# Optimization experiments

Measured on AMD Instinct MI355X. Metric: run time of the kernel, lower is better.

## Reference

```python
import jax, jax.numpy as jnp
import numpy as np

E4M3_MAX = 448.0  # fp8_max_fwd for Format.HYBRID fprop tensors
MARGIN = 0        # DelayedScaling default


def _quantize_e4m3(t, s):
    # cast_to_fp8: scale, saturate-cast to E4M3; amax of the unscaled tensor
    q = (t * s).astype(jnp.float8_e4m3fn)
    amax = jnp.max(jnp.abs(t))
    return q, amax


def _sf_compute(amax, scale, fp8_max, margin):
    # faithful port of _default_sf_compute (including its tf.where ordering)
    exp = jnp.floor(jnp.log2(fp8_max / amax)) - margin
    sf = jnp.round(jnp.exp2(jnp.abs(exp)))
    sf = jnp.where(amax > 0.0, sf, scale)
    sf = jnp.where(jnp.isinf(amax), sf, scale)
    sf = jnp.where(exp < 0, 1.0 / sf, sf)
    return sf


def setup_inputs() -> dict:
    key = jax.random.key(0)
    k1, k2 = jax.random.split(key)
    M, K, N = 16384, 2048, 2048
    x = jax.random.normal(k1, (M, K), dtype=jnp.float32)
    kernel = jax.random.normal(k2, (K, N), dtype=jnp.float32) * 0.02
    scale = jnp.ones((2,), dtype=jnp.float32)
    scale_inv = jnp.ones((2,), dtype=jnp.float32)
    amax_history = jnp.zeros((1, 2), dtype=jnp.float32)
    return {"x": x, "kernel": kernel, "scale": scale,
            "scale_inv": scale_inv, "amax_history": amax_history}


def reference(x, kernel, scale, scale_inv, amax_history):
    # --- cast_to_fp8 for activation (index 0) and weight (index 1) ---
    x_q, amax_x = _quantize_e4m3(x, scale[0])          # [M, K] fp8
    w_q, amax_w = _quantize_e4m3(kernel.T, scale[1])   # [N, K] fp8 (B in row-major, gemm does B^T)
    new_scale_inv = jnp.stack([1.0 / scale[0], 1.0 / scale[1]])
    # record amaxes into most-recent slot of the history
    amax_history = amax_history.at[0, 0].set(amax_x).at[0, 1].set(amax_w)

    # --- fp8_matmul: D = (A * A_scale_inv) @ (B * B_scale_inv)^T ---
    out = jnp.matmul(x_q.astype(jnp.float32), w_q.astype(jnp.float32).T)
    out = out * (new_scale_inv[0] * new_scale_inv[1])  # [M, N]

    # --- fused_amax_and_scale_update (amax_compute_algo='most_recent') ---
    amax = amax_history[0]
    rolled = jnp.roll(amax_history, -1, axis=0).at[0].set(0.0)
    new_scale = _sf_compute(amax, scale, E4M3_MAX, MARGIN)
    return out, new_scale, rolled
```

## Files before the change

### kernel.cpp

```cpp
#include <hip/hip_runtime.h>
#include <cstdint>

#define M_DIM 16384
#define K_DIM 2048
#define N_DIM 2048

typedef float f32x4 __attribute__((ext_vector_type(4)));
typedef int   i32x8 __attribute__((ext_vector_type(8)));

__global__ __launch_bounds__(256) void quant_x_kernel(
    const float4* __restrict__ x, uint4* __restrict__ xq,
    const float* __restrict__ scale, unsigned int* __restrict__ amax)
{
    const int gid = blockIdx.x * 256 + threadIdx.x;
    const float s = scale[0];
    float m = 0.0f;
#pragma unroll
    for (int j = 0; j < 8; ++j) {
        float4 v = x[gid + j * 1048576];
        m = fmaxf(m, fmaxf(fmaxf(fabsf(v.x), fabsf(v.y)),
                           fmaxf(fabsf(v.z), fabsf(v.w))));
        unsigned int p0 = __builtin_amdgcn_cvt_pk_fp8_f32(v.x * s, v.y * s, 0, false);
        unsigned int p  = __builtin_amdgcn_cvt_pk_fp8_f32(v.z * s, v.w * s, p0, true);
        ((unsigned int*)xq)[gid + j * 1048576] = p;
    }

#pragma unroll
    for (int off = 32; off > 0; off >>= 1)
        m = fmaxf(m, __shfl_down(m, off, 64));
    __shared__ float red[4];
    if ((threadIdx.x & 63) == 0) red[threadIdx.x >> 6] = m;
    __syncthreads();
    if (threadIdx.x == 0) {
        m = fmaxf(fmaxf(red[0], red[1]), fmaxf(red[2], red[3]));
        atomicMax(amax, __float_as_uint(m));
    }
}

__global__ __launch_bounds__(256) void quant_w_kernel(
    const float* __restrict__ w, uint8_t* __restrict__ wq,
    const float* __restrict__ scale, unsigned int* __restrict__ amax)
{
    __shared__ float tile[64][68];
    const int t = threadIdx.x;
    const int nb = blockIdx.x * 64;
    const int kb = blockIdx.y * 64;
    const float s = scale[1];
    float m = 0.0f;
#pragma unroll
    for (int j = 0; j < 4; ++j) {
        int f = j * 256 + t;
        int row = f >> 4;
        int c4 = f & 15;
        float4 v = *(const float4*)(w + (size_t)(kb + row) * N_DIM + nb + c4 * 4);
        m = fmaxf(m, fmaxf(fmaxf(fabsf(v.x), fabsf(v.y)),
                           fmaxf(fabsf(v.z), fabsf(v.w))));
        *(float4*)(&tile[row][c4 * 4]) = v;
    }
    __syncthreads();
    const int n = t >> 2, c = t & 3;
    unsigned int pk[4];
#pragma unroll
    for (int jj = 0; jj < 4; ++jj) {
        float f0 = tile[c * 16 + jj * 4 + 0][n] * s;
        float f1 = tile[c * 16 + jj * 4 + 1][n] * s;
        float f2 = tile[c * 16 + jj * 4 + 2][n] * s;
        float f3 = tile[c * 16 + jj * 4 + 3][n] * s;
        unsigned int p = __builtin_amdgcn_cvt_pk_fp8_f32(f0, f1, 0, false);
        pk[jj] = __builtin_amdgcn_cvt_pk_fp8_f32(f2, f3, p, true);
    }
    *(uint4*)(wq + (size_t)(nb + n) * K_DIM + kb + c * 16) = make_uint4(pk[0], pk[1], pk[2], pk[3]);

#pragma unroll
    for (int off = 32; off > 0; off >>= 1)
        m = fmaxf(m, __shfl_down(m, off, 64));
    __shared__ float red[4];
    if ((t & 63) == 0) red[t >> 6] = m;
    __syncthreads();
    if (t == 0) {
        m = fmaxf(fmaxf(red[0], red[1]), fmaxf(red[2], red[3]));
        atomicMax(amax, __float_as_uint(m));
    }
}

#define LDSBUF 32768

__global__ __launch_bounds__(512, 2) void gemm_fp8_kernel(
    const uint8_t* __restrict__ Aq, const uint8_t* __restrict__ Bq,
    const float* __restrict__ scale, float* __restrict__ C)
{
    extern __shared__ uint8_t lds[];
    uint8_t* const lA = lds;
    uint8_t* const lB = lds + 2 * LDSBUF;

    const int tid  = threadIdx.x;
    const int wave = tid >> 6;
    const int lane = tid & 63;
    const int wm = wave >> 2, wn = wave & 3;
    const int q = lane >> 4, r = lane & 15;

    const int bn = blockIdx.x;
    const int bm = blockIdx.y;

    const float s0 = scale[0];
    const float s1 = scale[1];
    asm volatile("s_waitcnt vmcnt(0) lgkmcnt(0)" ::: "memory");

    const int seg = wave & 1;
    const int wp  = wave >> 1;
    const int gbB = wp + ((wp >> 1) << 1);
    const int npr = seg * 64 + lane;
    const int nin = npr ^ ((npr >> 3) & 1);
    const int srow = (nin >> 1) & 15;
    const int skb  = (((nin >> 1) >> 4) << 5) + ((nin & 1) << 4);
    const int sdst = seg * 1024 + lane * 16;

    const uint8_t* aS = Aq + (size_t)(bm * 256 + srow) * K_DIM + skb;
    const uint8_t* bS = Bq + (size_t)(bn * 256 + srow) * K_DIM + skb;

#define STAGE_A(buf, kb, g)                                                          \
    __builtin_amdgcn_global_load_lds(                                                \
        (const __attribute__((address_space(1))) uint32_t*)(aS + (size_t)(g) * (16 * K_DIM) + (kb)), \
        (__attribute__((address_space(3))) uint32_t*)(lA + (buf) * LDSBUF + (g) * 2048 + sdst), 16, 0, 0)
#define STAGE_B(buf, kb, g)                                                          \
    __builtin_amdgcn_global_load_lds(                                                \
        (const __attribute__((address_space(1))) uint32_t*)(bS + (size_t)(g) * (16 * K_DIM) + (kb)), \
        (__attribute__((address_space(3))) uint32_t*)(lB + (buf) * LDSBUF + (g) * 2048 + sdst), 16, 0, 0)

    const int sb   = (lane >> 2) & 1;
    const int offL = (((lane << 1) ^ sb) << 4);
    const int offH = ((((lane << 1) + 1) ^ sb) << 4);

    f32x4 acc[8][4];
#pragma unroll
    for (int i = 0; i < 8; ++i)
#pragma unroll
        for (int j = 0; j < 4; ++j) acc[i][j] = (f32x4){0.f, 0.f, 0.f, 0.f};

    STAGE_A(0, 0, wp);       STAGE_A(0, 0, 8 + wp);
    STAGE_B(0, 0, gbB);      STAGE_B(0, 0, 8 + gbB);
    STAGE_B(0, 0, 2 + gbB);  STAGE_B(0, 0, 10 + gbB);
    STAGE_A(0, 0, 4 + wp);   STAGE_A(0, 0, 12 + wp);
    asm volatile("s_waitcnt vmcnt(4)" ::: "memory");
    __builtin_amdgcn_s_barrier();

    const int SONE = 0x7F7F7F7F;

#pragma unroll 2
    for (int t = 0; t < 16; ++t) {
        const int cur = t & 1, nxt = cur ^ 1;
        const int kbn = ((t + 1) & 15) * 128;
        uint8_t* const curA = lA + cur * LDSBUF;
        uint8_t* const curB = lB + cur * LDSBUF;
        i32x8 a_frag[4];
#pragma unroll
        for (int p = 0; p < 4; ++p) {
            const int mh = p >> 1, nh = p & 1;
            if (nh == 0) {
#pragma unroll
                for (int mi = 0; mi < 4; ++mi) {
                    const uint8_t* pa = curA + (wm * 8 + mh * 4 + mi) * 2048;
                    int4 lo = *(const int4*)(pa + offL);
                    int4 hi = *(const int4*)(pa + offH);
                    a_frag[mi] = (i32x8){lo.x, lo.y, lo.z, lo.w,
                                         hi.x, hi.y, hi.z, hi.w};
                }
            }
            i32x8 b_frag[2];
#pragma unroll
            for (int j = 0; j < 2; ++j) {
                const uint8_t* pb = curB + (wn * 4 + nh * 2 + j) * 2048;
                int4 lo = *(const int4*)(pb + offL);
                int4 hi = *(const int4*)(pb + offH);
                b_frag[j] = (i32x8){lo.x, lo.y, lo.z, lo.w,
                                    hi.x, hi.y, hi.z, hi.w};
            }
            if (p == 0)      { STAGE_A(nxt, kbn, wp);       STAGE_A(nxt, kbn, 8 + wp); }
            else if (p == 1) { STAGE_B(nxt, kbn, gbB);      STAGE_B(nxt, kbn, 8 + gbB); }
            else if (p == 2) { STAGE_B(nxt, kbn, 2 + gbB);  STAGE_B(nxt, kbn, 10 + gbB); }
            else             { STAGE_A(nxt, kbn, 4 + wp);   STAGE_A(nxt, kbn, 12 + wp); }

            if (p != 2) asm volatile("s_waitcnt vmcnt(4)" ::: "memory");
            __builtin_amdgcn_s_barrier();
            asm volatile("s_waitcnt lgkmcnt(0)" ::: "memory");
            __builtin_amdgcn_sched_barrier(0);
            __builtin_amdgcn_s_setprio(1);
#pragma unroll
            for (int mi = 0; mi < 4; ++mi)
#pragma unroll
                for (int j = 0; j < 2; ++j)
                    acc[mh * 4 + mi][nh * 2 + j] =
                        __builtin_amdgcn_mfma_scale_f32_16x16x128_f8f6f4(
                            a_frag[mi], b_frag[j], acc[mh * 4 + mi][nh * 2 + j],
                            0 , 0 ,
                            0, SONE, 0, SONE);
            __builtin_amdgcn_s_setprio(0);
            __builtin_amdgcn_s_barrier();
        }
    }
#undef STAGE_A
#undef STAGE_B

    const float sinv = (1.0f / s0) * (1.0f / s1);
#pragma unroll
    for (int mi = 0; mi < 8; ++mi) {
#pragma unroll
        for (int ni = 0; ni < 4; ++ni) {
            const int col  = bn * 256 + wn * 64 + ni * 16 + r;
            const int row0 = bm * 256 + wm * 128 + mi * 16 + q * 4;
#pragma unroll
            for (int rr = 0; rr < 4; ++rr)
                C[(size_t)(row0 + rr) * N_DIM + col] = acc[mi][ni][rr] * sinv;
        }
    }
}

__global__ void finalize_kernel(const float* __restrict__ scale,
                                const unsigned int* __restrict__ amax_bits,
                                float* __restrict__ out_tail)
{
    const int i = threadIdx.x;
    if (i < 2) {
        const float amax = __uint_as_float(amax_bits[i]);
        const float sc = scale[i];
        const float e = floorf(log2f(448.0f / amax));
        float sf = roundf(exp2f(fabsf(e)));
        sf = (amax > 0.0f) ? sf : sc;
        sf = isinf(amax) ? sf : sc;
        if (e < 0.0f) sf = 1.0f / sf;
        out_tail[i] = sf;
        out_tail[2 + i] = 0.0f;
    }
}

extern "C" void kernel_launch(void* const* d_in, const int* in_sizes, int n_in,
                              void* d_out, int out_size, void* d_ws, size_t ws_size,
                              hipStream_t stream)
{
    const float* x     = (const float*)d_in[0];
    const float* w     = (const float*)d_in[1];
    const float* scale = (const float*)d_in[2];

    uint8_t* ws = (uint8_t*)d_ws;
    uint8_t* xq = ws;
    uint8_t* wq = ws + (size_t)M_DIM * K_DIM;
    unsigned int* amax = (unsigned int*)(ws + (size_t)M_DIM * K_DIM + (size_t)N_DIM * K_DIM);

    static int lds_opt_in = 0;
    if (!lds_opt_in) {
        hipFuncSetAttribute((const void*)gemm_fp8_kernel,
                            hipFuncAttributeMaxDynamicSharedMemorySize, 131072);
        lds_opt_in = 1;
    }

    hipMemsetAsync(amax, 0, 2 * sizeof(unsigned int), stream);

    quant_x_kernel<<<4096, 256, 0, stream>>>(
        (const float4*)x, (uint4*)xq, scale, amax);

    dim3 gw(N_DIM / 64, K_DIM / 64);
    quant_w_kernel<<<gw, 256, 0, stream>>>(w, wq, scale, amax + 1);

    dim3 gg(N_DIM / 256, M_DIM / 256);
    gemm_fp8_kernel<<<gg, 512, 131072, stream>>>(xq, wq, scale, (float*)d_out);

    finalize_kernel<<<1, 64, 0, stream>>>(scale, amax,
                                          (float*)d_out + (size_t)M_DIM * N_DIM);
}
```

Baseline: 376.6 us.

## Restructure fp8 GEMM pipeline, add XCD-aware tile mapping, widen quant stores

Reorganizes the GEMM main loop: all next-tile loads are issued up front, and the four compute phases are split with finer vmcnt waits and fewer barriers. This reduces synchronization stalls. Blocks use a 1D grid remapped so each XCD gets contiguous M-tiles, to improve L2 reuse of B. The activation quantization now packs 16 values per thread into one 128-bit store, doubling the grid. The hand-tuned vmcnt counts risk subtle races if they are miscounted.

New measurement: 848.4 us. 125% more time.

```diff
diff --git a/kernel.cpp b/kernel.cpp
--- a/kernel.cpp
+++ b/kernel.cpp
@@ -14,16 +14,21 @@
 {
     const int gid = blockIdx.x * 256 + threadIdx.x;
     const float s = scale[0];
+    float4 vv[4];
+#pragma unroll
+    for (int j = 0; j < 4; ++j) vv[j] = x[gid * 4 + j];
+
     float m = 0.0f;
-#pragma unroll
-    for (int j = 0; j < 8; ++j) {
-        float4 v = x[gid + j * 1048576];
+    unsigned int pks[4];
+#pragma unroll
+    for (int j = 0; j < 4; ++j) {
+        float4 v = vv[j];
         m = fmaxf(m, fmaxf(fmaxf(fabsf(v.x), fabsf(v.y)),
                            fmaxf(fabsf(v.z), fabsf(v.w))));
         unsigned int p0 = __builtin_amdgcn_cvt_pk_fp8_f32(v.x * s, v.y * s, 0, false);
-        unsigned int p  = __builtin_amdgcn_cvt_pk_fp8_f32(v.z * s, v.w * s, p0, true);
-        ((unsigned int*)xq)[gid + j * 1048576] = p;
-    }
+        pks[j] = __builtin_amdgcn_cvt_pk_fp8_f32(v.z * s, v.w * s, p0, true);
+    }
+    xq[gid] = make_uint4(pks[0], pks[1], pks[2], pks[3]);
 
 #pragma unroll
     for (int off = 32; off > 0; off >>= 1)
@@ -99,8 +104,10 @@
     const int wm = wave >> 2, wn = wave & 3;
     const int q = lane >> 4, r = lane & 15;
 
-    const int bn = blockIdx.x;
-    const int bm = blockIdx.y;
+    const int id  = blockIdx.x;
+    const int xcd = id & 7, idx = id >> 3;
+    const int bm  = (xcd << 3) | (idx & 7);
+    const int bn  = idx >> 3;
 
     const float s0 = scale[0];
     const float s1 = scale[1];
@@ -131,6 +138,15 @@
     const int offL = (((lane << 1) ^ sb) << 4);
     const int offH = ((((lane << 1) + 1) ^ sb) << 4);
 
+#define LDA(mi, g) { const uint8_t* pa = curA + (g) * 2048;                 \
+        int4 lo = *(const int4*)(pa + offL);                                \
+        int4 hi = *(const int4*)(pa + offH);                                \
+        a_frag[mi] = (i32x8){lo.x,lo.y,lo.z,lo.w,hi.x,hi.y,hi.z,hi.w}; }
+#define LDB(j, g) { const uint8_t* pb = curB + (g) * 2048;                  \
+        int4 lo = *(const int4*)(pb + offL);                                \
+        int4 hi = *(const int4*)(pb + offH);                                \
+        b_frag[j] = (i32x8){lo.x,lo.y,lo.z,lo.w,hi.x,hi.y,hi.z,hi.w}; }
+
     f32x4 acc[8][4];
 #pragma unroll
     for (int i = 0; i < 8; ++i)
@@ -149,57 +165,72 @@
 #pragma unroll 2
     for (int t = 0; t < 16; ++t) {
         const int cur = t & 1, nxt = cur ^ 1;
-        const int kbn = ((t + 1) & 15) * 128;
+        const int kbn = (t + 1) * 128;
         uint8_t* const curA = lA + cur * LDSBUF;
         uint8_t* const curB = lB + cur * LDSBUF;
-        i32x8 a_frag[4];
-#pragma unroll
-        for (int p = 0; p < 4; ++p) {
-            const int mh = p >> 1, nh = p & 1;
-            if (nh == 0) {
-#pragma unroll
-                for (int mi = 0; mi < 4; ++mi) {
-                    const uint8_t* pa = curA + (wm * 8 + mh * 4 + mi) * 2048;
-                    int4 lo = *(const int4*)(pa + offL);
-                    int4 hi = *(const int4*)(pa + offH);
-                    a_frag[mi] = (i32x8){lo.x, lo.y, lo.z, lo.w,
-                                         hi.x, hi.y, hi.z, hi.w};
-                }
-            }
-            i32x8 b_frag[2];
-#pragma unroll
-            for (int j = 0; j < 2; ++j) {
-                const uint8_t* pb = curB + (wn * 4 + nh * 2 + j) * 2048;
-                int4 lo = *(const int4*)(pb + offL);
-                int4 hi = *(const int4*)(pb + offH);
-                b_frag[j] = (i32x8){lo.x, lo.y, lo.z, lo.w,
-                                    hi.x, hi.y, hi.z, hi.w};
-            }
-            if (p == 0)      { STAGE_A(nxt, kbn, wp);       STAGE_A(nxt, kbn, 8 + wp); }
-            else if (p == 1) { STAGE_B(nxt, kbn, gbB);      STAGE_B(nxt, kbn, 8 + gbB); }
-            else if (p == 2) { STAGE_B(nxt, kbn, 2 + gbB);  STAGE_B(nxt, kbn, 10 + gbB); }
-            else             { STAGE_A(nxt, kbn, 4 + wp);   STAGE_A(nxt, kbn, 12 + wp); }
-
-            if (p != 2) asm volatile("s_waitcnt vmcnt(4)" ::: "memory");
-            __builtin_amdgcn_s_barrier();
-            asm volatile("s_waitcnt lgkmcnt(0)" ::: "memory");
-            __builtin_amdgcn_sched_barrier(0);
-            __builtin_amdgcn_s_setprio(1);
-#pragma unroll
-            for (int mi = 0; mi < 4; ++mi)
-#pragma unroll
-                for (int j = 0; j < 2; ++j)
-                    acc[mh * 4 + mi][nh * 2 + j] =
-                        __builtin_amdgcn_mfma_scale_f32_16x16x128_f8f6f4(
-                            a_frag[mi], b_frag[j], acc[mh * 4 + mi][nh * 2 + j],
-                            0 , 0 ,
-                            0, SONE, 0, SONE);
-            __builtin_amdgcn_s_setprio(0);
-            __builtin_amdgcn_s_barrier();
+        i32x8 a_frag[4], b_frag[2];
+
+        LDA(0, wm * 8 + 0)  LDA(1, wm * 8 + 1)
+        LDA(2, wm * 8 + 2)  LDA(3, wm * 8 + 3)
+        LDB(0, wn * 4 + 0)  LDB(1, wn * 4 + 1)
+        if (t < 15) {
+            STAGE_A(nxt, kbn, wp);       STAGE_A(nxt, kbn, 8 + wp);
+            STAGE_B(nxt, kbn, gbB);      STAGE_B(nxt, kbn, 8 + gbB);
+            STAGE_B(nxt, kbn, 2 + gbB);  STAGE_B(nxt, kbn, 10 + gbB);
+            STAGE_A(nxt, kbn, 4 + wp);   STAGE_A(nxt, kbn, 12 + wp);
         }
+        __builtin_amdgcn_s_setprio(1);
+#pragma unroll
+        for (int mi = 0; mi < 4; ++mi)
+#pragma unroll
+            for (int j = 0; j < 2; ++j)
+                acc[mi][j] = __builtin_amdgcn_mfma_scale_f32_16x16x128_f8f6f4(
+                    a_frag[mi], b_frag[j], acc[mi][j], 0, 0, 0, SONE, 0, SONE);
+        __builtin_amdgcn_s_setprio(0);
+        if (t < 15) asm volatile("s_waitcnt vmcnt(10)" ::: "memory");
+        else        asm volatile("s_waitcnt vmcnt(2)"  ::: "memory");
+        __builtin_amdgcn_s_barrier();
+
+        LDB(0, wn * 4 + 2)  LDB(1, wn * 4 + 3)
+        __builtin_amdgcn_s_setprio(1);
+#pragma unroll
+        for (int mi = 0; mi < 4; ++mi)
+#pragma unroll
+            for (int j = 0; j < 2; ++j)
+                acc[mi][2 + j] = __builtin_amdgcn_mfma_scale_f32_16x16x128_f8f6f4(
+                    a_frag[mi], b_frag[j], acc[mi][2 + j], 0, 0, 0, SONE, 0, SONE);
+        __builtin_amdgcn_s_setprio(0);
+        if (t < 15) asm volatile("s_waitcnt vmcnt(8)" ::: "memory");
+        else        asm volatile("s_waitcnt vmcnt(0)" ::: "memory");
+        __builtin_amdgcn_s_barrier();
+
+        LDA(0, wm * 8 + 4)  LDA(1, wm * 8 + 5)
+        LDA(2, wm * 8 + 6)  LDA(3, wm * 8 + 7)
+        LDB(0, wn * 4 + 0)  LDB(1, wn * 4 + 1)
+        __builtin_amdgcn_s_setprio(1);
+#pragma unroll
+        for (int mi = 0; mi < 4; ++mi)
+#pragma unroll
+            for (int j = 0; j < 2; ++j)
+                acc[4 + mi][j] = __builtin_amdgcn_mfma_scale_f32_16x16x128_f8f6f4(
+                    a_frag[mi], b_frag[j], acc[4 + mi][j], 0, 0, 0, SONE, 0, SONE);
+        __builtin_amdgcn_s_setprio(0);
+        LDB(0, wn * 4 + 2)  LDB(1, wn * 4 + 3)
+        __builtin_amdgcn_s_setprio(1);
+#pragma unroll
+        for (int mi = 0; mi < 4; ++mi)
+#pragma unroll
+            for (int j = 0; j < 2; ++j)
+                acc[4 + mi][2 + j] = __builtin_amdgcn_mfma_scale_f32_16x16x128_f8f6f4(
+                    a_frag[mi], b_frag[j], acc[4 + mi][2 + j], 0, 0, 0, SONE, 0, SONE);
+        __builtin_amdgcn_s_setprio(0);
+        if (t < 15) asm volatile("s_waitcnt vmcnt(4)" ::: "memory");
+        __builtin_amdgcn_s_barrier();
     }
 #undef STAGE_A
 #undef STAGE_B
+#undef LDA
+#undef LDB
 
     const float sinv = (1.0f / s0) * (1.0f / s1);
 #pragma unroll
@@ -255,14 +286,13 @@
 
     hipMemsetAsync(amax, 0, 2 * sizeof(unsigned int), stream);
 
-    quant_x_kernel<<<4096, 256, 0, stream>>>(
+    quant_x_kernel<<<8192, 256, 0, stream>>>(
         (const float4*)x, (uint4*)xq, scale, amax);
 
     dim3 gw(N_DIM / 64, K_DIM / 64);
     quant_w_kernel<<<gw, 256, 0, stream>>>(w, wq, scale, amax + 1);
 
-    dim3 gg(N_DIM / 256, M_DIM / 256);
-    gemm_fp8_kernel<<<gg, 512, 131072, stream>>>(xq, wq, scale, (float*)d_out);
+    gemm_fp8_kernel<<<512, 512, 131072, stream>>>(xq, wq, scale, (float*)d_out);
 
     finalize_kernel<<<1, 64, 0, stream>>>(scale, amax,
                                           (float*)d_out + (size_t)M_DIM * N_DIM);
```
